# Optimization experiments

Measured on AMD Instinct MI355X. Metric: run time of the kernel, lower is better.

Reference implementation:

```python
import jax, jax.numpy as jnp
import numpy as np

B = 8192          # num_envs
OPT = 16          # num options
SHARED = 22       # shared_state_size (hardcoded in module)
UNIQ = 8          # unique_state_size (hardcoded in module)
MIN_DUR, MAX_DUR = 0.1, 0.5  # const.gait_net.valid_swing_duration_range


def _w(k, o, i):
    return jax.random.normal(k, (o, i), jnp.float32) * (1.0 / np.sqrt(i))


def setup_inputs() -> dict:
    key = jax.random.key(0)
    ks = jax.random.split(key, 20)
    obs = jax.random.normal(ks[0], (B, SHARED + OPT * UNIQ), jnp.float32)
    flag = jax.random.uniform(ks[1], (B, OPT)) < 0.25
    u = obs[:, SHARED:].reshape(B, OPT, UNIQ)
    u = u.at[:, :, 0].set(jnp.where(flag, 1.0, u[:, :, 0]))
    obs = jnp.concatenate([obs[:, :SHARED], u.reshape(B, OPT * UNIQ)], axis=1)
    return {
        "obs": obs,
        "sw1": _w(ks[2], 256, 22), "sb1": jnp.zeros((256,), jnp.float32),
        "sw2": _w(ks[3], 256, 256), "sb2": jnp.zeros((256,), jnp.float32),
        "uw1": _w(ks[4], 128, 8), "ub1": jnp.zeros((128,), jnp.float32),
        "uw2": _w(ks[5], 128, 128), "ub2": jnp.zeros((128,), jnp.float32),
        "no_op_embedding": jax.random.normal(ks[6], (128,), jnp.float32),
        "tw1": _w(ks[7], 512, 384), "tb1": jnp.zeros((512,), jnp.float32),
        "tw2": _w(ks[8], 256, 512), "tb2": jnp.zeros((256,), jnp.float32),
        "vw": _w(ks[9], 1, 256), "vb": jnp.zeros((1,), jnp.float32),
        "dw": _w(ks[10], 1, 256), "db": jnp.zeros((1,), jnp.float32),
    }


def reference(obs, sw1, sb1, sw2, sb2, uw1, ub1, uw2, ub2, no_op_embedding,
              tw1, tb1, tw2, tb2, vw, vb, dw, db):
    relu = jax.nn.relu
    shared = obs[:, :SHARED]                               # [B, 22]
    uniq = obs[:, SHARED:].reshape(B, OPT, UNIQ)           # [B, OPT, 8]
    # shared encoder (22 -> 256 -> 256, relu output)
    se = relu(relu(shared @ sw1.T + sb1) @ sw2.T + sb2)    # [B, 256]
    # unique encoder applied to all options at once (8 -> 128 -> 128)
    ue = relu(relu(uniq @ uw1.T + ub1) @ uw2.T + ub2)      # [B, OPT, 128]
    no_op = uniq[:, :, 0] == 1.0                           # [B, OPT]
    ue = jnp.where(no_op[..., None], no_op_embedding, ue)
    trunk_in = jnp.concatenate(
        [jnp.broadcast_to(se[:, None, :], (B, OPT, se.shape[-1])), ue], axis=-1)
    t = relu(relu(trunk_in @ tw1.T + tb1) @ tw2.T + tb2)   # [B, OPT, 256]
    logits = (t @ vw.T + vb).squeeze(-1)                   # [B, OPT]
    duration = jax.nn.sigmoid((t @ dw.T + db).squeeze(-1)) * (MAX_DUR - MIN_DUR) + MIN_DUR
    return logits, duration
```

## Files before the change

kernel.cpp:

```cpp
#include <hip/hip_runtime.h>
#include <stdint.h>


static constexpr int B_ = 8192;

typedef __attribute__((ext_vector_type(8))) short bf16x8;
typedef __attribute__((ext_vector_type(4))) float f32x4;

__device__ __forceinline__ float u2f(uint16_t u) {
    union { uint32_t i; float f; } c; c.i = (uint32_t)u << 16; return c.f;
}
__device__ __forceinline__ uint16_t f2u(float f) {
    __bf16 b = (__bf16)f;
    return __builtin_bit_cast(uint16_t, b);
}
__device__ __forceinline__ ushort4 pack4(float a, float b, float c, float d) {
    ushort4 o;
    o.x = f2u(a); o.y = f2u(b); o.z = f2u(c); o.w = f2u(d);
    return o;
}

static constexpr size_t WCSE   = 0;
static constexpr size_t WTW1SE = 4194304;
static constexpr size_t WTW1UE = WTW1SE + 131072;
static constexpr size_t WTW2   = WTW1UE + 65536;
static constexpr size_t WUW2   = WTW2 + 131072;
static constexpr size_t WSW2   = WUW2 + 16384;
static constexpr size_t WUW1B  = WSW2 + 65536;

__global__ __launch_bounds__(256) void k_conv(
    const float* __restrict__ tw1, const float* __restrict__ tw2,
    const float* __restrict__ uw2, const float* __restrict__ sw2,
    const float* __restrict__ uw1, uint16_t* __restrict__ ws)
{
    int i4 = blockIdx.x * 256 + threadIdx.x;
    if (i4 >= 102400) {
        int q = i4 - 102400;
        int n = q >> 3, k0 = (q & 7) * 4;
        ushort4 o = {0, 0, 0, 0};
        if (k0 < 8) {
            float4 v = *reinterpret_cast<const float4*>(uw1 + n * 8 + k0);
            o.x = f2u(v.x); o.y = f2u(v.y); o.z = f2u(v.z); o.w = f2u(v.w);
        }
        *reinterpret_cast<ushort4*>(ws + WUW1B + n * 32 + k0) = o;
        return;
    }
    const float* src; size_t dst;
    if (i4 < 32768) {
        int g = i4 * 4, n = g >> 8, k = g & 255;
        src = tw1 + (size_t)n * 384 + k;
        dst = WTW1SE + (size_t)g;
    } else if (i4 < 49152) {
        int q = i4 - 32768, n = q >> 5, w = q & 31;
        src = tw1 + (size_t)n * 384 + 256 + w * 4;
        dst = WTW1UE + (size_t)n * 128 + w * 4;
    } else if (i4 < 81920) {
        int q = (i4 - 49152) * 4;
        src = tw2 + q; dst = WTW2 + q;
    } else if (i4 < 86016) {
        int q = (i4 - 81920) * 4;
        src = uw2 + q; dst = WUW2 + q;
    } else {
        int q = (i4 - 86016) * 4;
        src = sw2 + q; dst = WSW2 + q;
    }
    float4 v = *reinterpret_cast<const float4*>(src);
    ushort4 o;
    o.x = f2u(v.x); o.y = f2u(v.y); o.z = f2u(v.z); o.w = f2u(v.w);
    *reinterpret_cast<ushort4*>(ws + dst) = o;
}

__global__ __launch_bounds__(512) void k_cse(
    const float* __restrict__ obs,
    const float* __restrict__ sw1, const float* __restrict__ sb1,
    const float* __restrict__ sb2, const float* __restrict__ tb1,
    uint16_t* __restrict__ ws)
{
    __shared__ float xs[16][24];
    __shared__ uint16_t h1s[16 * 264];
    __shared__ uint16_t seL[16 * 264];
    const int t = threadIdx.x;
    const int b0 = blockIdx.x * 16;
    const int wv = t >> 6, lane = t & 63, quad = lane >> 4, l16 = lane & 15;
    const uint16_t* sw2b   = ws + WSW2;
    const uint16_t* tw1seb = ws + WTW1SE;

    if (t < 352) {
        int e = t / 22, c = t - e * 22;
        xs[e][c] = obs[(size_t)(b0 + e) * 150 + c];
    }
    __syncthreads();
    const uint16_t* bb_se = sw2b + (size_t)(wv * 32 + l16) * 256 + quad * 8;
    bf16x8 seb0 = *reinterpret_cast<const bf16x8*>(bb_se);
    bf16x8 seb1 = *reinterpret_cast<const bf16x8*>(bb_se + 4096);
    {
        const int n = t & 255;
        float w[22];
        #pragma unroll
        for (int k = 0; k < 22; ++k) w[k] = sw1[n * 22 + k];
        const float bias = sb1[n];
        #pragma unroll
        for (int ii = 0; ii < 8; ++ii) {
            int e = (t >> 8) * 8 + ii;
            float a = bias;
            #pragma unroll
            for (int k = 0; k < 22; ++k) a += w[k] * xs[e][k];
            h1s[e * 264 + n] = f2u(fmaxf(a, 0.f));
        }
    }
    __syncthreads();
    const uint16_t* bb_c = tw1seb + (size_t)(wv * 64 + l16) * 256 + quad * 8;
    bf16x8 cseb[4];
    #pragma unroll
    for (int nt = 0; nt < 4; ++nt)
        cseb[nt] = *reinterpret_cast<const bf16x8*>(bb_c + nt * 4096);
    {
        f32x4 acc[2];
        #pragma unroll
        for (int nt = 0; nt < 2; ++nt) {
            float bv = sb2[wv * 32 + nt * 16 + l16];
            acc[nt] = {bv, bv, bv, bv};
        }
        bf16x8 bc[2], bn[2];
        bc[0] = seb0; bc[1] = seb1;
        #pragma unroll
        for (int kk = 0; kk < 8; ++kk) {
            if (kk < 7) {
                bn[0] = *reinterpret_cast<const bf16x8*>(bb_se + (kk + 1) * 32);
                bn[1] = *reinterpret_cast<const bf16x8*>(bb_se + 4096 + (kk + 1) * 32);
            }
            bf16x8 af = *reinterpret_cast<const bf16x8*>(
                &h1s[l16 * 264 + kk * 32 + quad * 8]);
            #pragma unroll
            for (int nt = 0; nt < 2; ++nt)
                acc[nt] = __builtin_amdgcn_mfma_f32_16x16x32_bf16(
                    af, bc[nt], acc[nt], 0, 0, 0);
            bc[0] = bn[0]; bc[1] = bn[1];
        }
        #pragma unroll
        for (int nt = 0; nt < 2; ++nt)
            #pragma unroll
            for (int r = 0; r < 4; ++r)
                seL[(quad * 4 + r) * 264 + wv * 32 + nt * 16 + l16] =
                    f2u(fmaxf(acc[nt][r], 0.f));
    }
    __syncthreads();
    {
        f32x4 acc[4];
        #pragma unroll
        for (int nt = 0; nt < 4; ++nt) {
            float bv = tb1[wv * 64 + nt * 16 + l16];
            acc[nt] = {bv, bv, bv, bv};
        }
        bf16x8 bc[4], bn[4];
        #pragma unroll
        for (int nt = 0; nt < 4; ++nt) bc[nt] = cseb[nt];
        #pragma unroll
        for (int kk = 0; kk < 8; ++kk) {
            if (kk < 7) {
                #pragma unroll
                for (int nt = 0; nt < 4; ++nt)
                    bn[nt] = *reinterpret_cast<const bf16x8*>(
                        bb_c + nt * 4096 + (kk + 1) * 32);
            }
            bf16x8 af = *reinterpret_cast<const bf16x8*>(
                &seL[l16 * 264 + kk * 32 + quad * 8]);
            #pragma unroll
            for (int nt = 0; nt < 4; ++nt)
                acc[nt] = __builtin_amdgcn_mfma_f32_16x16x32_bf16(
                    af, bc[nt], acc[nt], 0, 0, 0);
            #pragma unroll
            for (int nt = 0; nt < 4; ++nt) bc[nt] = bn[nt];
        }
        #pragma unroll
        for (int nt = 0; nt < 4; ++nt)
            #pragma unroll
            for (int r = 0; r < 4; ++r)
                ws[WCSE + (size_t)(b0 + quad * 4 + r) * 512 +
                   wv * 64 + nt * 16 + l16] = f2u(acc[nt][r]);
    }
}

static constexpr int UQB_OFF  = 0;
static constexpr int NOOP_OFF = 5120;
static constexpr int CSE_OFF  = 5376;
static constexpr int H1U_OFF  = 9472;
static constexpr int UET_OFF  = 26880;
static constexpr int H1T_OFF  = 44288;
static constexpr int SMEM_SZ  = 78080;

__global__ __launch_bounds__(512, 4) void k_main(
    const float* __restrict__ obs,
    const float* __restrict__ ub1,
    const float* __restrict__ ub2, const float* __restrict__ emb,
    const float* __restrict__ tb2,
    const float* __restrict__ vw,  const float* __restrict__ vb,
    const float* __restrict__ dw,  const float* __restrict__ db,
    const uint16_t* __restrict__ wsb,
    float* __restrict__ out)
{
    __shared__ __align__(16) char smem[SMEM_SZ];
    uint16_t* uqb   = (uint16_t*)(smem + UQB_OFF);
    float*    noopf = (float*)(smem + NOOP_OFF);
    uint16_t* cseL  = (uint16_t*)(smem + CSE_OFF);
    uint16_t* h1u   = (uint16_t*)(smem + H1U_OFF);
    uint16_t* uet   = (uint16_t*)(smem + UET_OFF);
    uint16_t* h1t   = (uint16_t*)(smem + H1T_OFF);
    float*    hred  = (float*)(smem + H1T_OFF);

    const int t    = threadIdx.x;
    const int wv   = t >> 6;
    const int lane = t & 63;
    const int quad = lane >> 4;
    const int l16  = lane & 15;
    const int b0   = blockIdx.x * 4;

    const uint16_t* csep  = wsb + WCSE;
    const uint16_t* tw1ue = wsb + WTW1UE;
    const uint16_t* tw2b  = wsb + WTW2;
    const uint16_t* uw2b  = wsb + WUW2;
    const uint16_t* uw1b  = wsb + WUW1B;

    uint32_t cse_r0, cse_r1;
    bf16x8 wf2;
    {
        int r = t >> 3, q = t & 7;
        int e = r >> 4, o = r & 15;
        ushort4 ov = {0, 0, 0, 0};
        if (q < 2) {
            const float2* sp = reinterpret_cast<const float2*>(
                &obs[(size_t)(b0 + e) * 150 + 22 + o * 8 + q * 4]);
            float2 a = sp[0], b = sp[1];
            ov.x = f2u(a.x); ov.y = f2u(a.y); ov.z = f2u(b.x); ov.w = f2u(b.y);
        }
        *reinterpret_cast<ushort4*>(&uqb[r * 40 + q * 4]) = ov;
        const uint32_t* cp = (const uint32_t*)(csep + (size_t)b0 * 512);
        cse_r0 = cp[t];
        cse_r1 = cp[t + 512];
        wf2 = *reinterpret_cast<const bf16x8*>(
            &uw1b[(wv * 16 + l16) * 32 + quad * 8]);
        if (t < 64) {
            int ee = t >> 4, oo = t & 15;
            noopf[t] = (obs[(size_t)(b0 + ee) * 150 + 22 + oo * 8] == 1.0f) ? 1.0f : 0.0f;
        }
    }
    __syncthreads();

    bf16x8 wf3;
    {
        float4 bv4 = *reinterpret_cast<const float4*>(&ub1[wv * 16 + quad * 4]);
        f32x4 acc[4];
        #pragma unroll
        for (int mt = 0; mt < 4; ++mt) acc[mt] = {bv4.x, bv4.y, bv4.z, bv4.w};
        #pragma unroll
        for (int mt = 0; mt < 4; ++mt) {
            bf16x8 xf = *reinterpret_cast<const bf16x8*>(
                &uqb[(mt * 16 + l16) * 40 + quad * 8]);
            acc[mt] = __builtin_amdgcn_mfma_f32_16x16x32_bf16(wf2, xf, acc[mt], 0, 0, 0);
        }
        wf3 = *reinterpret_cast<const bf16x8*>(
            &uw2b[(size_t)(wv * 16 + l16) * 128 + quad * 8]);
        #pragma unroll
        for (int mt = 0; mt < 4; ++mt) {
            ushort4 o = pack4(fmaxf(acc[mt][0], 0.f), fmaxf(acc[mt][1], 0.f),
                              fmaxf(acc[mt][2], 0.f), fmaxf(acc[mt][3], 0.f));
            *reinterpret_cast<ushort4*>(
                &h1u[(mt * 16 + l16) * 136 + wv * 16 + quad * 4]) = o;
        }
    }
    __syncthreads();

    {
        float4 bv4 = *reinterpret_cast<const float4*>(&ub2[wv * 16 + quad * 4]);
        float4 ev4 = *reinterpret_cast<const float4*>(&emb[wv * 16 + quad * 4]);
        f32x4 acc[4];
        #pragma unroll
        for (int mt = 0; mt < 4; ++mt) acc[mt] = {bv4.x, bv4.y, bv4.z, bv4.w};
        bf16x8 wfc = wf3, wfn;
        #pragma unroll
        for (int kk = 0; kk < 4; ++kk) {
            if (kk < 3)
                wfn = *reinterpret_cast<const bf16x8*>(
                    &uw2b[(size_t)(wv * 16 + l16) * 128 + (kk + 1) * 32 + quad * 8]);
            #pragma unroll
            for (int mt = 0; mt < 4; ++mt) {
                bf16x8 xf = *reinterpret_cast<const bf16x8*>(
                    &h1u[(mt * 16 + l16) * 136 + kk * 32 + quad * 8]);
                acc[mt] = __builtin_amdgcn_mfma_f32_16x16x32_bf16(wfc, xf, acc[mt], 0, 0, 0);
            }
            wfc = wfn;
        }
        #pragma unroll
        for (int mt = 0; mt < 4; ++mt) {
            bool noop = (noopf[mt * 16 + l16] != 0.0f);
            ushort4 o = pack4(noop ? ev4.x : fmaxf(acc[mt][0], 0.f),
                              noop ? ev4.y : fmaxf(acc[mt][1], 0.f),
                              noop ? ev4.z : fmaxf(acc[mt][2], 0.f),
                              noop ? ev4.w : fmaxf(acc[mt][3], 0.f));
            *reinterpret_cast<ushort4*>(
                &uet[(mt * 16 + l16) * 136 + wv * 16 + quad * 4]) = o;
        }
        ((uint32_t*)cseL)[t] = cse_r0;
        ((uint32_t*)cseL)[t + 512] = cse_r1;
    }
    __syncthreads();

    f32x4 acc2[4][2];
    #pragma unroll
    for (int nt = 0; nt < 2; ++nt) {
        float4 bv4 = *reinterpret_cast<const float4*>(
            &tb2[wv * 32 + nt * 16 + quad * 4]);
        #pragma unroll
        for (int mt = 0; mt < 4; ++mt) acc2[mt][nt] = {bv4.x, bv4.y, bv4.z, bv4.w};
    }

    const uint16_t* tw1ue_base = tw1ue + (size_t)(wv * 32 + l16) * 128 + quad * 8;
    bf16x8 bc[2], bn[2];
    bc[0] = *reinterpret_cast<const bf16x8*>(tw1ue_base);
    bc[1] = *reinterpret_cast<const bf16x8*>(tw1ue_base + 2048);

    #pragma unroll
    for (int nc = 0; nc < 2; ++nc) {
        const uint16_t* bb = tw1ue_base + (size_t)nc * 32768;
        const uint16_t* cb = tw2b + (size_t)(wv * 32 + l16) * 512 + nc * 256
                             + quad * 8;
        bf16x8 cc[2], cn[2];
        cc[0] = *reinterpret_cast<const bf16x8*>(cb);
        cc[1] = *reinterpret_cast<const bf16x8*>(cb + 8192);
        {
            f32x4 acc1[4][2];
            #pragma unroll
            for (int nt = 0; nt < 2; ++nt) {
                int n0 = nc * 256 + wv * 32 + nt * 16 + quad * 4;
                #pragma unroll
                for (int mt = 0; mt < 4; ++mt) {
                    ushort4 cv = *reinterpret_cast<const ushort4*>(
                        &cseL[mt * 512 + n0]);
                    acc1[mt][nt] = {u2f(cv.x), u2f(cv.y), u2f(cv.z), u2f(cv.w)};
                }
            }
            #pragma unroll
            for (int kk = 0; kk < 4; ++kk) {
                if (kk < 3) {
                    bn[0] = *reinterpret_cast<const bf16x8*>(bb + (kk + 1) * 32);
                    bn[1] = *reinterpret_cast<const bf16x8*>(bb + 2048 + (kk + 1) * 32);
                }
                bf16x8 af[4];
                #pragma unroll
                for (int mt = 0; mt < 4; ++mt)
                    af[mt] = *reinterpret_cast<const bf16x8*>(
                        &uet[(mt * 16 + l16) * 136 + kk * 32 + quad * 8]);
                #pragma unroll
                for (int mt = 0; mt < 4; ++mt)
                    #pragma unroll
                    for (int nt = 0; nt < 2; ++nt)
                        acc1[mt][nt] = __builtin_amdgcn_mfma_f32_16x16x32_bf16(
                            bc[nt], af[mt], acc1[mt][nt], 0, 0, 0);
                bc[0] = bn[0]; bc[1] = bn[1];
            }
            if (nc == 0) {
                bc[0] = *reinterpret_cast<const bf16x8*>(tw1ue_base + 32768);
                bc[1] = *reinterpret_cast<const bf16x8*>(tw1ue_base + 32768 + 2048);
            }
            #pragma unroll
            for (int mt = 0; mt < 4; ++mt)
                #pragma unroll
                for (int nt = 0; nt < 2; ++nt) {
                    ushort4 o = pack4(fmaxf(acc1[mt][nt][0], 0.f),
                                      fmaxf(acc1[mt][nt][1], 0.f),
                                      fmaxf(acc1[mt][nt][2], 0.f),
                                      fmaxf(acc1[mt][nt][3], 0.f));
                    *reinterpret_cast<ushort4*>(
                        &h1t[(mt * 16 + l16) * 264 + wv * 32 + nt * 16 + quad * 4]) = o;
                }
        }
        __syncthreads();
        {
            #pragma unroll
            for (int k2 = 0; k2 < 8; ++k2) {
                if (k2 < 7) {
                    cn[0] = *reinterpret_cast<const bf16x8*>(cb + (k2 + 1) * 32);
                    cn[1] = *reinterpret_cast<const bf16x8*>(cb + 8192 + (k2 + 1) * 32);
                }
                bf16x8 af[4];
                #pragma unroll
                for (int mt = 0; mt < 4; ++mt)
                    af[mt] = *reinterpret_cast<const bf16x8*>(
                        &h1t[(mt * 16 + l16) * 264 + k2 * 32 + quad * 8]);
                #pragma unroll
                for (int mt = 0; mt < 4; ++mt)
                    #pragma unroll
                    for (int nt = 0; nt < 2; ++nt)
                        acc2[mt][nt] = __builtin_amdgcn_mfma_f32_16x16x32_bf16(
                            cc[nt], af[mt], acc2[mt][nt], 0, 0, 0);
                cc[0] = cn[0]; cc[1] = cn[1];
            }
        }
        if (nc == 0) __syncthreads();
    }
    __syncthreads();

    {
        float svr[4] = {0.f, 0.f, 0.f, 0.f};
        float sdr[4] = {0.f, 0.f, 0.f, 0.f};
        #pragma unroll
        for (int nt = 0; nt < 2; ++nt) {
            float4 vw4 = *reinterpret_cast<const float4*>(
                &vw[wv * 32 + nt * 16 + quad * 4]);
            float4 dw4 = *reinterpret_cast<const float4*>(
                &dw[wv * 32 + nt * 16 + quad * 4]);
            #pragma unroll
            for (int mt = 0; mt < 4; ++mt) {
                float t0 = fmaxf(acc2[mt][nt][0], 0.f);
                float t1 = fmaxf(acc2[mt][nt][1], 0.f);
                float t2 = fmaxf(acc2[mt][nt][2], 0.f);
                float t3 = fmaxf(acc2[mt][nt][3], 0.f);
                svr[mt] += t0 * vw4.x + t1 * vw4.y + t2 * vw4.z + t3 * vw4.w;
                sdr[mt] += t0 * dw4.x + t1 * dw4.y + t2 * dw4.z + t3 * dw4.w;
            }
        }
        #pragma unroll
        for (int mt = 0; mt < 4; ++mt) {
            svr[mt] += __shfl_xor(svr[mt], 16);
            svr[mt] += __shfl_xor(svr[mt], 32);
            sdr[mt] += __shfl_xor(sdr[mt], 16);
            sdr[mt] += __shfl_xor(sdr[mt], 32);
        }
        if (quad == 0) {
            #pragma unroll
            for (int mt = 0; mt < 4; ++mt) {
                int row = mt * 16 + l16;
                hred[(row * 2 + 0) * 8 + wv] = svr[mt];
                hred[(row * 2 + 1) * 8 + wv] = sdr[mt];
            }
        }
    }
    __syncthreads();
    if (t < 128) {
        const float* p = &hred[t * 8];
        float s = p[0] + p[1] + p[2] + p[3] + p[4] + p[5] + p[6] + p[7];
        int row = t >> 1;
        int g = blockIdx.x * 64 + row;
        if ((t & 1) == 0) {
            out[g] = s + vb[0];
        } else {
            float z = s + db[0];
            float sig = 1.f / (1.f + __expf(-z));
            out[B_ * 16 + g] = sig * 0.4f + 0.1f;
        }
    }
}

extern "C" void kernel_launch(void* const* d_in, const int* in_sizes, int n_in,
                              void* d_out, int out_size, void* d_ws, size_t ws_size,
                              hipStream_t stream) {
    const float* obs = (const float*)d_in[0];
    const float* sw1 = (const float*)d_in[1];
    const float* sb1 = (const float*)d_in[2];
    const float* sw2 = (const float*)d_in[3];
    const float* sb2 = (const float*)d_in[4];
    const float* uw1 = (const float*)d_in[5];
    const float* ub1 = (const float*)d_in[6];
    const float* uw2 = (const float*)d_in[7];
    const float* ub2 = (const float*)d_in[8];
    const float* emb = (const float*)d_in[9];
    const float* tw1 = (const float*)d_in[10];
    const float* tb1 = (const float*)d_in[11];
    const float* tw2 = (const float*)d_in[12];
    const float* tb2 = (const float*)d_in[13];
    const float* vw  = (const float*)d_in[14];
    const float* vb  = (const float*)d_in[15];
    const float* dw  = (const float*)d_in[16];
    const float* db  = (const float*)d_in[17];

    uint16_t* wsb = (uint16_t*)d_ws;

    k_conv<<<404, 256, 0, stream>>>(tw1, tw2, uw2, sw2, uw1, wsb);
    k_cse<<<512, 512, 0, stream>>>(obs, sw1, sb1, sb2, tb1, wsb);
    k_main<<<B_ / 4, 512, 0, stream>>>(obs, ub1, ub2, emb, tb2,
                                       vw, vb, dw, db, wsb, (float*)d_out);
}
```

Baseline: 222.4 us.

## Fuse shared-encoder kernel into main kernel, processing 16 envs per block

```diff
diff --git a/kernel.cpp b/kernel.cpp
--- a/kernel.cpp
+++ b/kernel.cpp
@@ -20,7 +20,6 @@
     return o;
 }
 
-static constexpr size_t WCSE   = 0;
 static constexpr size_t WTW1SE = 4194304;
 static constexpr size_t WTW1UE = WTW1SE + 131072;
 static constexpr size_t WTW2   = WTW1UE + 65536;
@@ -70,127 +69,22 @@
     *reinterpret_cast<ushort4*>(ws + dst) = o;
 }
 
-__global__ __launch_bounds__(512) void k_cse(
+static constexpr int CSE_OFF  = 0;
+static constexpr int UET_OFF  = 16384;
+static constexpr int H1T_OFF  = 33792;
+static constexpr int H1U_OFF  = 33792;
+static constexpr int H1S_OFF  = 33792;
+static constexpr int SEL_OFF  = 42240;
+static constexpr int XS_OFF   = 50688;
+static constexpr int UQB_OFF  = 67584;
+static constexpr int NOOP_OFF = 72704;
+static constexpr int HRED_OFF = 72960;
+static constexpr int SMEM_SZ  = 77056;
+
+__global__ __launch_bounds__(512, 4) void k_fused(
     const float* __restrict__ obs,
     const float* __restrict__ sw1, const float* __restrict__ sb1,
     const float* __restrict__ sb2, const float* __restrict__ tb1,
-    uint16_t* __restrict__ ws)
-{
-    __shared__ float xs[16][24];
-    __shared__ uint16_t h1s[16 * 264];
-    __shared__ uint16_t seL[16 * 264];
-    const int t = threadIdx.x;
-    const int b0 = blockIdx.x * 16;
-    const int wv = t >> 6, lane = t & 63, quad = lane >> 4, l16 = lane & 15;
-    const uint16_t* sw2b   = ws + WSW2;
-    const uint16_t* tw1seb = ws + WTW1SE;
-
-    if (t < 352) {
-        int e = t / 22, c = t - e * 22;
-        xs[e][c] = obs[(size_t)(b0 + e) * 150 + c];
-    }
-    __syncthreads();
-    const uint16_t* bb_se = sw2b + (size_t)(wv * 32 + l16) * 256 + quad * 8;
-    bf16x8 seb0 = *reinterpret_cast<const bf16x8*>(bb_se);
-    bf16x8 seb1 = *reinterpret_cast<const bf16x8*>(bb_se + 4096);
-    {
-        const int n = t & 255;
-        float w[22];
-        #pragma unroll
-        for (int k = 0; k < 22; ++k) w[k] = sw1[n * 22 + k];
-        const float bias = sb1[n];
-        #pragma unroll
-        for (int ii = 0; ii < 8; ++ii) {
-            int e = (t >> 8) * 8 + ii;
-            float a = bias;
-            #pragma unroll
-            for (int k = 0; k < 22; ++k) a += w[k] * xs[e][k];
-            h1s[e * 264 + n] = f2u(fmaxf(a, 0.f));
-        }
-    }
-    __syncthreads();
-    const uint16_t* bb_c = tw1seb + (size_t)(wv * 64 + l16) * 256 + quad * 8;
-    bf16x8 cseb[4];
-    #pragma unroll
-    for (int nt = 0; nt < 4; ++nt)
-        cseb[nt] = *reinterpret_cast<const bf16x8*>(bb_c + nt * 4096);
-    {
-        f32x4 acc[2];
-        #pragma unroll
-        for (int nt = 0; nt < 2; ++nt) {
-            float bv = sb2[wv * 32 + nt * 16 + l16];
-            acc[nt] = {bv, bv, bv, bv};
-        }
-        bf16x8 bc[2], bn[2];
-        bc[0] = seb0; bc[1] = seb1;
-        #pragma unroll
-        for (int kk = 0; kk < 8; ++kk) {
-            if (kk < 7) {
-                bn[0] = *reinterpret_cast<const bf16x8*>(bb_se + (kk + 1) * 32);
-                bn[1] = *reinterpret_cast<const bf16x8*>(bb_se + 4096 + (kk + 1) * 32);
-            }
-            bf16x8 af = *reinterpret_cast<const bf16x8*>(
-                &h1s[l16 * 264 + kk * 32 + quad * 8]);
-            #pragma unroll
-            for (int nt = 0; nt < 2; ++nt)
-                acc[nt] = __builtin_amdgcn_mfma_f32_16x16x32_bf16(
-                    af, bc[nt], acc[nt], 0, 0, 0);
-            bc[0] = bn[0]; bc[1] = bn[1];
-        }
-        #pragma unroll
-        for (int nt = 0; nt < 2; ++nt)
-            #pragma unroll
-            for (int r = 0; r < 4; ++r)
-                seL[(quad * 4 + r) * 264 + wv * 32 + nt * 16 + l16] =
-                    f2u(fmaxf(acc[nt][r], 0.f));
-    }
-    __syncthreads();
-    {
-        f32x4 acc[4];
-        #pragma unroll
-        for (int nt = 0; nt < 4; ++nt) {
-            float bv = tb1[wv * 64 + nt * 16 + l16];
-            acc[nt] = {bv, bv, bv, bv};
-        }
-        bf16x8 bc[4], bn[4];
-        #pragma unroll
-        for (int nt = 0; nt < 4; ++nt) bc[nt] = cseb[nt];
-        #pragma unroll
-        for (int kk = 0; kk < 8; ++kk) {
-            if (kk < 7) {
-                #pragma unroll
-                for (int nt = 0; nt < 4; ++nt)
-                    bn[nt] = *reinterpret_cast<const bf16x8*>(
-                        bb_c + nt * 4096 + (kk + 1) * 32);
-            }
-            bf16x8 af = *reinterpret_cast<const bf16x8*>(
-                &seL[l16 * 264 + kk * 32 + quad * 8]);
-            #pragma unroll
-            for (int nt = 0; nt < 4; ++nt)
-                acc[nt] = __builtin_amdgcn_mfma_f32_16x16x32_bf16(
-                    af, bc[nt], acc[nt], 0, 0, 0);
-            #pragma unroll
-            for (int nt = 0; nt < 4; ++nt) bc[nt] = bn[nt];
-        }
-        #pragma unroll
-        for (int nt = 0; nt < 4; ++nt)
-            #pragma unroll
-            for (int r = 0; r < 4; ++r)
-                ws[WCSE + (size_t)(b0 + quad * 4 + r) * 512 +
-                   wv * 64 + nt * 16 + l16] = f2u(acc[nt][r]);
-    }
-}
-
-static constexpr int UQB_OFF  = 0;
-static constexpr int NOOP_OFF = 5120;
-static constexpr int CSE_OFF  = 5376;
-static constexpr int H1U_OFF  = 9472;
-static constexpr int UET_OFF  = 26880;
-static constexpr int H1T_OFF  = 44288;
-static constexpr int SMEM_SZ  = 78080;
-
-__global__ __launch_bounds__(512, 4) void k_main(
-    const float* __restrict__ obs,
     const float* __restrict__ ub1,
     const float* __restrict__ ub2, const float* __restrict__ emb,
     const float* __restrict__ tb2,
@@ -200,253 +94,376 @@
     float* __restrict__ out)
 {
     __shared__ __align__(16) char smem[SMEM_SZ];
+    uint16_t* cseL  = (uint16_t*)(smem + CSE_OFF);
+    uint16_t* uet   = (uint16_t*)(smem + UET_OFF);
+    uint16_t* h1t   = (uint16_t*)(smem + H1T_OFF);
+    uint16_t* h1u   = (uint16_t*)(smem + H1U_OFF);
+    uint16_t* h1s   = (uint16_t*)(smem + H1S_OFF);
+    uint16_t* seL   = (uint16_t*)(smem + SEL_OFF);
+    float*    xs    = (float*)(smem + XS_OFF);
     uint16_t* uqb   = (uint16_t*)(smem + UQB_OFF);
     float*    noopf = (float*)(smem + NOOP_OFF);
-    uint16_t* cseL  = (uint16_t*)(smem + CSE_OFF);
-    uint16_t* h1u   = (uint16_t*)(smem + H1U_OFF);
-    uint16_t* uet   = (uint16_t*)(smem + UET_OFF);
-    uint16_t* h1t   = (uint16_t*)(smem + H1T_OFF);
-    float*    hred  = (float*)(smem + H1T_OFF);
+    float*    hred  = (float*)(smem + HRED_OFF);
 
     const int t    = threadIdx.x;
     const int wv   = t >> 6;
     const int lane = t & 63;
     const int quad = lane >> 4;
     const int l16  = lane & 15;
-    const int b0   = blockIdx.x * 4;
-
-    const uint16_t* csep  = wsb + WCSE;
-    const uint16_t* tw1ue = wsb + WTW1UE;
-    const uint16_t* tw2b  = wsb + WTW2;
-    const uint16_t* uw2b  = wsb + WUW2;
-    const uint16_t* uw1b  = wsb + WUW1B;
-
-    uint32_t cse_r0, cse_r1;
-    bf16x8 wf2;
+    const int bb16 = blockIdx.x * 16;
+
+    const uint16_t* tw1seb = wsb + WTW1SE;
+    const uint16_t* tw1ue  = wsb + WTW1UE;
+    const uint16_t* tw2b   = wsb + WTW2;
+    const uint16_t* uw2b   = wsb + WUW2;
+    const uint16_t* sw2b   = wsb + WSW2;
+    const uint16_t* uw1b   = wsb + WUW1B;
+
+    const int ur = t >> 3, uq = t & 7;
+    const int ue_ = ur >> 4, uo = ur & 15;
+
     {
-        int r = t >> 3, q = t & 7;
-        int e = r >> 4, o = r & 15;
+        if (t < 352) {
+            int e = t / 22, c = t - e * 22;
+            xs[e * 24 + c] = obs[(size_t)(bb16 + e) * 150 + c];
+        }
         ushort4 ov = {0, 0, 0, 0};
-        if (q < 2) {
+        if (uq < 2) {
             const float2* sp = reinterpret_cast<const float2*>(
-                &obs[(size_t)(b0 + e) * 150 + 22 + o * 8 + q * 4]);
+                &obs[(size_t)(bb16 + ue_) * 150 + 22 + uo * 8 + uq * 4]);
             float2 a = sp[0], b = sp[1];
             ov.x = f2u(a.x); ov.y = f2u(a.y); ov.z = f2u(b.x); ov.w = f2u(b.y);
         }
-        *reinterpret_cast<ushort4*>(&uqb[r * 40 + q * 4]) = ov;
-        const uint32_t* cp = (const uint32_t*)(csep + (size_t)b0 * 512);
-        cse_r0 = cp[t];
-        cse_r1 = cp[t + 512];
-        wf2 = *reinterpret_cast<const bf16x8*>(
-            &uw1b[(wv * 16 + l16) * 32 + quad * 8]);
+        *reinterpret_cast<ushort4*>(&uqb[ur * 40 + uq * 4]) = ov;
         if (t < 64) {
             int ee = t >> 4, oo = t & 15;
-            noopf[t] = (obs[(size_t)(b0 + ee) * 150 + 22 + oo * 8] == 1.0f) ? 1.0f : 0.0f;
+            noopf[t] = (obs[(size_t)(bb16 + ee) * 150 + 22 + oo * 8] == 1.0f)
+                           ? 1.0f : 0.0f;
         }
     }
     __syncthreads();
-
-    bf16x8 wf3;
+    const uint16_t* bb_se = sw2b + (size_t)(wv * 32 + l16) * 256 + quad * 8;
+    bf16x8 seb0 = *reinterpret_cast<const bf16x8*>(bb_se);
+    bf16x8 seb1 = *reinterpret_cast<const bf16x8*>(bb_se + 4096);
     {
-        float4 bv4 = *reinterpret_cast<const float4*>(&ub1[wv * 16 + quad * 4]);
+        const int n = t & 255;
+        float w[22];
+        #pragma unroll
+        for (int k = 0; k < 22; ++k) w[k] = sw1[n * 22 + k];
+        const float bias = sb1[n];
+        #pragma unroll
+        for (int ii = 0; ii < 8; ++ii) {
+            int e = (t >> 8) * 8 + ii;
+            float a = bias;
+            #pragma unroll
+            for (int k = 0; k < 22; ++k) a += w[k] * xs[e * 24 + k];
+            h1s[e * 264 + n] = f2u(fmaxf(a, 0.f));
+        }
+    }
+    __syncthreads();
+    const uint16_t* bb_c = tw1seb + (size_t)(wv * 64 + l16) * 256 + quad * 8;
+    bf16x8 cseb[4];
+    #pragma unroll
+    for (int nt = 0; nt < 4; ++nt)
+        cseb[nt] = *reinterpret_cast<const bf16x8*>(bb_c + nt * 4096);
+    {
+        f32x4 acc[2];
+        #pragma unroll
+        for (int nt = 0; nt < 2; ++nt) {
+            float bv = sb2[wv * 32 + nt * 16 + l16];
+            acc[nt] = {bv, bv, bv, bv};
+        }
+        bf16x8 bc[2], bn[2];
+        bc[0] = seb0; bc[1] = seb1;
+        #pragma unroll
+        for (int kk = 0; kk < 8; ++kk) {
+            if (kk < 7) {
+                bn[0] = *reinterpret_cast<const bf16x8*>(bb_se + (kk + 1) * 32);
+                bn[1] = *reinterpret_cast<const bf16x8*>(bb_se + 4096 + (kk + 1) * 32);
+            }
+            bf16x8 af = *reinterpret_cast<const bf16x8*>(
+                &h1s[l16 * 264 + kk * 32 + quad * 8]);
+            #pragma unroll
+            for (int nt = 0; nt < 2; ++nt)
+                acc[nt] = __builtin_amdgcn_mfma_f32_16x16x32_bf16(
+                    af, bc[nt], acc[nt], 0, 0, 0);
+            bc[0] = bn[0]; bc[1] = bn[1];
+        }
+        #pragma unroll
+        for (int nt = 0; nt < 2; ++nt)
+            #pragma unroll
+            for (int r = 0; r < 4; ++r)
+                seL[(quad * 4 + r) * 264 + wv * 32 + nt * 16 + l16] =
+                    f2u(fmaxf(acc[nt][r], 0.f));
+    }
+    __syncthreads();
+    {
         f32x4 acc[4];
         #pragma unroll
-        for (int mt = 0; mt < 4; ++mt) acc[mt] = {bv4.x, bv4.y, bv4.z, bv4.w};
-        #pragma unroll
-        for (int mt = 0; mt < 4; ++mt) {
-            bf16x8 xf = *reinterpret_cast<const bf16x8*>(
-                &uqb[(mt * 16 + l16) * 40 + quad * 8]);
-            acc[mt] = __builtin_amdgcn_mfma_f32_16x16x32_bf16(wf2, xf, acc[mt], 0, 0, 0);
-        }
-        wf3 = *reinterpret_cast<const bf16x8*>(
-            &uw2b[(size_t)(wv * 16 + l16) * 128 + quad * 8]);
-        #pragma unroll
-        for (int mt = 0; mt < 4; ++mt) {
-            ushort4 o = pack4(fmaxf(acc[mt][0], 0.f), fmaxf(acc[mt][1], 0.f),
-                              fmaxf(acc[mt][2], 0.f), fmaxf(acc[mt][3], 0.f));
-            *reinterpret_cast<ushort4*>(
-                &h1u[(mt * 16 + l16) * 136 + wv * 16 + quad * 4]) = o;
-        }
+        for (int nt = 0; nt < 4; ++nt) {
+            float bv = tb1[wv * 64 + nt * 16 + l16];
+            acc[nt] = {bv, bv, bv, bv};
+        }
+        bf16x8 bc[4], bn[4];
+        #pragma unroll
+        for (int nt = 0; nt < 4; ++nt) bc[nt] = cseb[nt];
+        #pragma unroll
+        for (int kk = 0; kk < 8; ++kk) {
+            if (kk < 7) {
+                #pragma unroll
+                for (int nt = 0; nt < 4; ++nt)
+                    bn[nt] = *reinterpret_cast<const bf16x8*>(
+                        bb_c + nt * 4096 + (kk + 1) * 32);
+            }
+            bf16x8 af = *reinterpret_cast<const bf16x8*>(
+                &seL[l16 * 264 + kk * 32 + quad * 8]);
+            #pragma unroll
+            for (int nt = 0; nt < 4; ++nt)
+                acc[nt] = __builtin_amdgcn_mfma_f32_16x16x32_bf16(
+                    af, bc[nt], acc[nt], 0, 0, 0);
+            #pragma unroll
+            for (int nt = 0; nt < 4; ++nt) bc[nt] = bn[nt];
+        }
+        #pragma unroll
+        for (int nt = 0; nt < 4; ++nt)
+            #pragma unroll
+            for (int r = 0; r < 4; ++r)
+                cseL[(quad * 4 + r) * 512 + wv * 64 + nt * 16 + l16] =
+                    f2u(acc[nt][r]);
     }
     __syncthreads();
 
-    {
-        float4 bv4 = *reinterpret_cast<const float4*>(&ub2[wv * 16 + quad * 4]);
-        float4 ev4 = *reinterpret_cast<const float4*>(&emb[wv * 16 + quad * 4]);
-        f32x4 acc[4];
-        #pragma unroll
-        for (int mt = 0; mt < 4; ++mt) acc[mt] = {bv4.x, bv4.y, bv4.z, bv4.w};
-        bf16x8 wfc = wf3, wfn;
-        #pragma unroll
-        for (int kk = 0; kk < 4; ++kk) {
-            if (kk < 3)
-                wfn = *reinterpret_cast<const bf16x8*>(
-                    &uw2b[(size_t)(wv * 16 + l16) * 128 + (kk + 1) * 32 + quad * 8]);
+    const uint16_t* tw1ue_base = tw1ue + (size_t)(wv * 32 + l16) * 128 + quad * 8;
+    bf16x8 wf2 = *reinterpret_cast<const bf16x8*>(
+        &uw1b[(wv * 16 + l16) * 32 + quad * 8]);
+
+    #pragma unroll 1
+    for (int c = 0; c < 4; ++c) {
+        const int b0c = bb16 + c * 4;
+
+        bf16x8 wf3;
+        {
+            float4 bv4 = *reinterpret_cast<const float4*>(&ub1[wv * 16 + quad * 4]);
+            f32x4 acc[4];
+            #pragma unroll
+            for (int mt = 0; mt < 4; ++mt) acc[mt] = {bv4.x, bv4.y, bv4.z, bv4.w};
             #pragma unroll
             for (int mt = 0; mt < 4; ++mt) {
                 bf16x8 xf = *reinterpret_cast<const bf16x8*>(
-                    &h1u[(mt * 16 + l16) * 136 + kk * 32 + quad * 8]);
-                acc[mt] = __builtin_amdgcn_mfma_f32_16x16x32_bf16(wfc, xf, acc[mt], 0, 0, 0);
-            }
-            wfc = wfn;
-        }
-        #pragma unroll
-        for (int mt = 0; mt < 4; ++mt) {
-            bool noop = (noopf[mt * 16 + l16] != 0.0f);
-            ushort4 o = pack4(noop ? ev4.x : fmaxf(acc[mt][0], 0.f),
-                              noop ? ev4.y : fmaxf(acc[mt][1], 0.f),
-                              noop ? ev4.z : fmaxf(acc[mt][2], 0.f),
-                              noop ? ev4.w : fmaxf(acc[mt][3], 0.f));
-            *reinterpret_cast<ushort4*>(
-                &uet[(mt * 16 + l16) * 136 + wv * 16 + quad * 4]) = o;
-        }
-        ((uint32_t*)cseL)[t] = cse_r0;
-        ((uint32_t*)cseL)[t + 512] = cse_r1;
-    }
-    __syncthreads();
-
-    f32x4 acc2[4][2];
-    #pragma unroll
-    for (int nt = 0; nt < 2; ++nt) {
-        float4 bv4 = *reinterpret_cast<const float4*>(
-            &tb2[wv * 32 + nt * 16 + quad * 4]);
-        #pragma unroll
-        for (int mt = 0; mt < 4; ++mt) acc2[mt][nt] = {bv4.x, bv4.y, bv4.z, bv4.w};
-    }
-
-    const uint16_t* tw1ue_base = tw1ue + (size_t)(wv * 32 + l16) * 128 + quad * 8;
-    bf16x8 bc[2], bn[2];
-    bc[0] = *reinterpret_cast<const bf16x8*>(tw1ue_base);
-    bc[1] = *reinterpret_cast<const bf16x8*>(tw1ue_base + 2048);
-
-    #pragma unroll
-    for (int nc = 0; nc < 2; ++nc) {
-        const uint16_t* bb = tw1ue_base + (size_t)nc * 32768;
-        const uint16_t* cb = tw2b + (size_t)(wv * 32 + l16) * 512 + nc * 256
-                             + quad * 8;
-        bf16x8 cc[2], cn[2];
-        cc[0] = *reinterpret_cast<const bf16x8*>(cb);
-        cc[1] = *reinterpret_cast<const bf16x8*>(cb + 8192);
+                    &uqb[(mt * 16 + l16) * 40 + quad * 8]);
+                acc[mt] = __builtin_amdgcn_mfma_f32_16x16x32_bf16(wf2, xf, acc[mt], 0, 0, 0);
+            }
+            wf3 = *reinterpret_cast<const bf16x8*>(
+                &uw2b[(size_t)(wv * 16 + l16) * 128 + quad * 8]);
+            #pragma unroll
+            for (int mt = 0; mt < 4; ++mt) {
+                ushort4 o = pack4(fmaxf(acc[mt][0], 0.f), fmaxf(acc[mt][1], 0.f),
+                                  fmaxf(acc[mt][2], 0.f), fmaxf(acc[mt][3], 0.f));
+                *reinterpret_cast<ushort4*>(
+                    &h1u[(mt * 16 + l16) * 136 + wv * 16 + quad * 4]) = o;
+            }
+        }
+        __syncthreads();
+
         {
-            f32x4 acc1[4][2];
+            float4 bv4 = *reinterpret_cast<const float4*>(&ub2[wv * 16 + quad * 4]);
+            float4 ev4 = *reinterpret_cast<const float4*>(&emb[wv * 16 + quad * 4]);
+            f32x4 acc[4];
+            #pragma unroll
+            for (int mt = 0; mt < 4; ++mt) acc[mt] = {bv4.x, bv4.y, bv4.z, bv4.w};
+            bf16x8 wfc = wf3, wfn;
+            #pragma unroll
+            for (int kk = 0; kk < 4; ++kk) {
+                if (kk < 3)
+                    wfn = *reinterpret_cast<const bf16x8*>(
+                        &uw2b[(size_t)(wv * 16 + l16) * 128 + (kk + 1) * 32 + quad * 8]);
+                #pragma unroll
+                for (int mt = 0; mt < 4; ++mt) {
+                    bf16x8 xf = *reinterpret_cast<const bf16x8*>(
+                        &h1u[(mt * 16 + l16) * 136 + kk * 32 + quad * 8]);
+                    acc[mt] = __builtin_amdgcn_mfma_f32_16x16x32_bf16(wfc, xf, acc[mt], 0, 0, 0);
+                }
+                wfc = wfn;
+            }
+            #pragma unroll
+            for (int mt = 0; mt < 4; ++mt) {
+                bool noop = (noopf[mt * 16 + l16] != 0.0f);
+                ushort4 o = pack4(noop ? ev4.x : fmaxf(acc[mt][0], 0.f),
+                                  noop ? ev4.y : fmaxf(acc[mt][1], 0.f),
+                                  noop ? ev4.z : fmaxf(acc[mt][2], 0.f),
+                                  noop ? ev4.w : fmaxf(acc[mt][3], 0.f));
+                *reinterpret_cast<ushort4*>(
+                    &uet[(mt * 16 + l16) * 136 + wv * 16 + quad * 4]) = o;
+            }
+        }
+        __syncthreads();
+
+        float2 pf_a, pf_b; float pf_noop = 0.f;
+        const bool havepf = (c < 3);
+        if (havepf) {
+            const int b0n = b0c + 4;
+            if (uq < 2) {
+                const float2* sp = reinterpret_cast<const float2*>(
+                    &obs[(size_t)(b0n + ue_) * 150 + 22 + uo * 8 + uq * 4]);
+                pf_a = sp[0]; pf_b = sp[1];
+            }
+            if (t < 64) {
+                int ee = t >> 4, oo = t & 15;
+                pf_noop = obs[(size_t)(b0n + ee) * 150 + 22 + oo * 8];
+            }
+        }
+
+        f32x4 acc2[4][2];
+        #pragma unroll
+        for (int nt = 0; nt < 2; ++nt) {
+            float4 bv4 = *reinterpret_cast<const float4*>(
+                &tb2[wv * 32 + nt * 16 + quad * 4]);
+            #pragma unroll
+            for (int mt = 0; mt < 4; ++mt) acc2[mt][nt] = {bv4.x, bv4.y, bv4.z, bv4.w};
+        }
+
+        bf16x8 bc[2], bn[2];
+        bc[0] = *reinterpret_cast<const bf16x8*>(tw1ue_base);
+        bc[1] = *reinterpret_cast<const bf16x8*>(tw1ue_base + 2048);
+
+        #pragma unroll
+        for (int nc = 0; nc < 2; ++nc) {
+            const uint16_t* bb = tw1ue_base + (size_t)nc * 32768;
+            const uint16_t* cb = tw2b + (size_t)(wv * 32 + l16) * 512 + nc * 256
+                                 + quad * 8;
+            bf16x8 cc[2], cn[2];
+            cc[0] = *reinterpret_cast<const bf16x8*>(cb);
+            cc[1] = *reinterpret_cast<const bf16x8*>(cb + 8192);
+            {
+                f32x4 acc1[4][2];
+                #pragma unroll
+                for (int nt = 0; nt < 2; ++nt) {
+                    int n0 = nc * 256 + wv * 32 + nt * 16 + quad * 4;
+                    #pragma unroll
+                    for (int mt = 0; mt < 4; ++mt) {
+                        ushort4 cv = *reinterpret_cast<const ushort4*>(
+                            &cseL[(c * 4 + mt) * 512 + n0]);
+                        acc1[mt][nt] = {u2f(cv.x), u2f(cv.y), u2f(cv.z), u2f(cv.w)};
+                    }
+                }
+                #pragma unroll
+                for (int kk = 0; kk < 4; ++kk) {
+                    if (kk < 3) {
+                        bn[0] = *reinterpret_cast<const bf16x8*>(bb + (kk + 1) * 32);
+                        bn[1] = *reinterpret_cast<const bf16x8*>(bb + 2048 + (kk + 1) * 32);
+                    }
+                    bf16x8 af[4];
+                    #pragma unroll
+                    for (int mt = 0; mt < 4; ++mt)
+                        af[mt] = *reinterpret_cast<const bf16x8*>(
+                            &uet[(mt * 16 + l16) * 136 + kk * 32 + quad * 8]);
+                    #pragma unroll
+                    for (int mt = 0; mt < 4; ++mt)
+                        #pragma unroll
+                        for (int nt = 0; nt < 2; ++nt)
+                            acc1[mt][nt] = __builtin_amdgcn_mfma_f32_16x16x32_bf16(
+                                bc[nt], af[mt], acc1[mt][nt], 0, 0, 0);
+                    bc[0] = bn[0]; bc[1] = bn[1];
+                }
+                if (nc == 0) {
+                    bc[0] = *reinterpret_cast<const bf16x8*>(tw1ue_base + 32768);
+                    bc[1] = *reinterpret_cast<const bf16x8*>(tw1ue_base + 32768 + 2048);
+                }
+                #pragma unroll
+                for (int mt = 0; mt < 4; ++mt)
+                    #pragma unroll
+                    for (int nt = 0; nt < 2; ++nt) {
+                        ushort4 o = pack4(fmaxf(acc1[mt][nt][0], 0.f),
+                                          fmaxf(acc1[mt][nt][1], 0.f),
+                                          fmaxf(acc1[mt][nt][2], 0.f),
+                                          fmaxf(acc1[mt][nt][3], 0.f));
+                        *reinterpret_cast<ushort4*>(
+                            &h1t[(mt * 16 + l16) * 264 + wv * 32 + nt * 16 + quad * 4]) = o;
+                    }
+            }
+            __syncthreads();
+            {
+                #pragma unroll
+                for (int k2 = 0; k2 < 8; ++k2) {
+                    if (k2 < 7) {
+                        cn[0] = *reinterpret_cast<const bf16x8*>(cb + (k2 + 1) * 32);
+                        cn[1] = *reinterpret_cast<const bf16x8*>(cb + 8192 + (k2 + 1) * 32);
+                    }
+                    bf16x8 af[4];
+                    #pragma unroll
+                    for (int mt = 0; mt < 4; ++mt)
+                        af[mt] = *reinterpret_cast<const bf16x8*>(
+                            &h1t[(mt * 16 + l16) * 264 + k2 * 32 + quad * 8]);
+                    #pragma unroll
+                    for (int mt = 0; mt < 4; ++mt)
+                        #pragma unroll
+                        for (int nt = 0; nt < 2; ++nt)
+                            acc2[mt][nt] = __builtin_amdgcn_mfma_f32_16x16x32_bf16(
+                                cc[nt], af[mt], acc2[mt][nt], 0, 0, 0);
+                    cc[0] = cn[0]; cc[1] = cn[1];
+                }
+            }
+            if (nc == 0) __syncthreads();
+        }
+        __syncthreads();
+
+        {
+            float svr[4] = {0.f, 0.f, 0.f, 0.f};
+            float sdr[4] = {0.f, 0.f, 0.f, 0.f};
             #pragma unroll
             for (int nt = 0; nt < 2; ++nt) {
-                int n0 = nc * 256 + wv * 32 + nt * 16 + quad * 4;
+                float4 vw4 = *reinterpret_cast<const float4*>(
+                    &vw[wv * 32 + nt * 16 + quad * 4]);
+                float4 dw4 = *reinterpret_cast<const float4*>(
+                    &dw[wv * 32 + nt * 16 + quad * 4]);
                 #pragma unroll
                 for (int mt = 0; mt < 4; ++mt) {
-                    ushort4 cv = *reinterpret_cast<const ushort4*>(
-                        &cseL[mt * 512 + n0]);
-                    acc1[mt][nt] = {u2f(cv.x), u2f(cv.y), u2f(cv.z), u2f(cv.w)};
-                }
-            }
-            #pragma unroll
-            for (int kk = 0; kk < 4; ++kk) {
-                if (kk < 3) {
-                    bn[0] = *reinterpret_cast<const bf16x8*>(bb + (kk + 1) * 32);
-                    bn[1] = *reinterpret_cast<const bf16x8*>(bb + 2048 + (kk + 1) * 32);
-                }
-                bf16x8 af[4];
-                #pragma unroll
-                for (int mt = 0; mt < 4; ++mt)
-                    af[mt] = *reinterpret_cast<const bf16x8*>(
-                        &uet[(mt * 16 + l16) * 136 + kk * 32 + quad * 8]);
-                #pragma unroll
-                for (int mt = 0; mt < 4; ++mt)
-                    #pragma unroll
-                    for (int nt = 0; nt < 2; ++nt)
-                        acc1[mt][nt] = __builtin_amdgcn_mfma_f32_16x16x32_bf16(
-                            bc[nt], af[mt], acc1[mt][nt], 0, 0, 0);
-                bc[0] = bn[0]; bc[1] = bn[1];
-            }
-            if (nc == 0) {
-                bc[0] = *reinterpret_cast<const bf16x8*>(tw1ue_base + 32768);
-                bc[1] = *reinterpret_cast<const bf16x8*>(tw1ue_base + 32768 + 2048);
-            }
-            #pragma unroll
-            for (int mt = 0; mt < 4; ++mt)
-                #pragma unroll
-                for (int nt = 0; nt < 2; ++nt) {
-                    ushort4 o = pack4(fmaxf(acc1[mt][nt][0], 0.f),
-                                      fmaxf(acc1[mt][nt][1], 0.f),
-                                      fmaxf(acc1[mt][nt][2], 0.f),
-                                      fmaxf(acc1[mt][nt][3], 0.f));
-                    *reinterpret_cast<ushort4*>(
-                        &h1t[(mt * 16 + l16) * 264 + wv * 32 + nt * 16 + quad * 4]) = o;
-                }
+                    float t0 = fmaxf(acc2[mt][nt][0], 0.f);
+                    float t1 = fmaxf(acc2[mt][nt][1], 0.f);
+                    float t2v = fmaxf(acc2[mt][nt][2], 0.f);
+                    float t3 = fmaxf(acc2[mt][nt][3], 0.f);
+                    svr[mt] += t0 * vw4.x + t1 * vw4.y + t2v * vw4.z + t3 * vw4.w;
+                    sdr[mt] += t0 * dw4.x + t1 * dw4.y + t2v * dw4.z + t3 * dw4.w;
+                }
+            }
+            #pragma unroll
+            for (int mt = 0; mt < 4; ++mt) {
+                svr[mt] += __shfl_xor(svr[mt], 16);
+                svr[mt] += __shfl_xor(svr[mt], 32);
+                sdr[mt] += __shfl_xor(sdr[mt], 16);
+                sdr[mt] += __shfl_xor(sdr[mt], 32);
+            }
+            if (quad == 0) {
+                #pragma unroll
+                for (int mt = 0; mt < 4; ++mt) {
+                    int row = mt * 16 + l16;
+                    hred[(row * 2 + 0) * 8 + wv] = svr[mt];
+                    hred[(row * 2 + 1) * 8 + wv] = sdr[mt];
+                }
+            }
+            if (havepf) {
+                ushort4 ov = {0, 0, 0, 0};
+                if (uq < 2) {
+                    ov.x = f2u(pf_a.x); ov.y = f2u(pf_a.y);
+                    ov.z = f2u(pf_b.x); ov.w = f2u(pf_b.y);
+                }
+                *reinterpret_cast<ushort4*>(&uqb[ur * 40 + uq * 4]) = ov;
+                if (t < 64) noopf[t] = (pf_noop == 1.0f) ? 1.0f : 0.0f;
+            }
         }
         __syncthreads();
-        {
-            #pragma unroll
-            for (int k2 = 0; k2 < 8; ++k2) {
-                if (k2 < 7) {
-                    cn[0] = *reinterpret_cast<const bf16x8*>(cb + (k2 + 1) * 32);
-                    cn[1] = *reinterpret_cast<const bf16x8*>(cb + 8192 + (k2 + 1) * 32);
-                }
-                bf16x8 af[4];
-                #pragma unroll
-                for (int mt = 0; mt < 4; ++mt)
-                    af[mt] = *reinterpret_cast<const bf16x8*>(
-                        &h1t[(mt * 16 + l16) * 264 + k2 * 32 + quad * 8]);
-                #pragma unroll
-                for (int mt = 0; mt < 4; ++mt)
-                    #pragma unroll
-                    for (int nt = 0; nt < 2; ++nt)
-                        acc2[mt][nt] = __builtin_amdgcn_mfma_f32_16x16x32_bf16(
-                            cc[nt], af[mt], acc2[mt][nt], 0, 0, 0);
-                cc[0] = cn[0]; cc[1] = cn[1];
-            }
-        }
-        if (nc == 0) __syncthreads();
-    }
-    __syncthreads();
-
-    {
-        float svr[4] = {0.f, 0.f, 0.f, 0.f};
-        float sdr[4] = {0.f, 0.f, 0.f, 0.f};
-        #pragma unroll
-        for (int nt = 0; nt < 2; ++nt) {
-            float4 vw4 = *reinterpret_cast<const float4*>(
-                &vw[wv * 32 + nt * 16 + quad * 4]);
-            float4 dw4 = *reinterpret_cast<const float4*>(
-                &dw[wv * 32 + nt * 16 + quad * 4]);
-            #pragma unroll
-            for (int mt = 0; mt < 4; ++mt) {
-                float t0 = fmaxf(acc2[mt][nt][0], 0.f);
-                float t1 = fmaxf(acc2[mt][nt][1], 0.f);
-                float t2 = fmaxf(acc2[mt][nt][2], 0.f);
-                float t3 = fmaxf(acc2[mt][nt][3], 0.f);
-                svr[mt] += t0 * vw4.x + t1 * vw4.y + t2 * vw4.z + t3 * vw4.w;
-                sdr[mt] += t0 * dw4.x + t1 * dw4.y + t2 * dw4.z + t3 * dw4.w;
-            }
-        }
-        #pragma unroll
-        for (int mt = 0; mt < 4; ++mt) {
-            svr[mt] += __shfl_xor(svr[mt], 16);
-            svr[mt] += __shfl_xor(svr[mt], 32);
-            sdr[mt] += __shfl_xor(sdr[mt], 16);
-            sdr[mt] += __shfl_xor(sdr[mt], 32);
-        }
-        if (quad == 0) {
-            #pragma unroll
-            for (int mt = 0; mt < 4; ++mt) {
-                int row = mt * 16 + l16;
-                hred[(row * 2 + 0) * 8 + wv] = svr[mt];
-                hred[(row * 2 + 1) * 8 + wv] = sdr[mt];
-            }
-        }
-    }
-    __syncthreads();
-    if (t < 128) {
-        const float* p = &hred[t * 8];
-        float s = p[0] + p[1] + p[2] + p[3] + p[4] + p[5] + p[6] + p[7];
-        int row = t >> 1;
-        int g = blockIdx.x * 64 + row;
-        if ((t & 1) == 0) {
-            out[g] = s + vb[0];
-        } else {
-            float z = s + db[0];
-            float sig = 1.f / (1.f + __expf(-z));
-            out[B_ * 16 + g] = sig * 0.4f + 0.1f;
+        if (t < 128) {
+            const float* p = &hred[t * 8];
+            float s = p[0] + p[1] + p[2] + p[3] + p[4] + p[5] + p[6] + p[7];
+            int row = t >> 1;
+            int g = blockIdx.x * 256 + c * 64 + row;
+            if ((t & 1) == 0) {
+                out[g] = s + vb[0];
+            } else {
+                float z = s + db[0];
+                float sig = 1.f / (1.f + __expf(-z));
+                out[B_ * 16 + g] = sig * 0.4f + 0.1f;
+            }
         }
     }
 }
@@ -476,7 +493,7 @@
     uint16_t* wsb = (uint16_t*)d_ws;
 
     k_conv<<<404, 256, 0, stream>>>(tw1, tw2, uw2, sw2, uw1, wsb);
-    k_cse<<<512, 512, 0, stream>>>(obs, sw1, sb1, sb2, tb1, wsb);
-    k_main<<<B_ / 4, 512, 0, stream>>>(obs, ub1, ub2, emb, tb2,
-                                       vw, vb, dw, db, wsb, (float*)d_out);
-}
+    k_fused<<<B_ / 16, 512, 0, stream>>>(obs, sw1, sb1, sb2, tb1,
+                                         ub1, ub2, emb, tb2,
+                                         vw, vb, dw, db, wsb, (float*)d_out);
+}
```

Result: slower. 397.1 us (+78.5%).
